# Performance work log

Hardware: AMD Instinct MI355X
Metric: run time of the kernel (lower is better)

The kernel has to match this reference:

```python
import jax, jax.numpy as jnp
import numpy as np

NUM_EXPERTS = 8
TOP_K = 2
B, T, D, F = 4, 2048, 1024, 2816


def setup_inputs() -> dict:
    key = jax.random.key(0)
    ks = jax.random.split(key, 5)
    return {
        "x": jax.random.normal(ks[0], (B, T, D), dtype=jnp.float32),
        "router_w": jax.random.normal(ks[1], (D, NUM_EXPERTS), dtype=jnp.float32) * 0.02,
        "gate_proj": jax.random.normal(ks[2], (NUM_EXPERTS, D, F), dtype=jnp.float32) * 0.02,
        "up_proj": jax.random.normal(ks[3], (NUM_EXPERTS, D, F), dtype=jnp.float32) * 0.02,
        "down_proj": jax.random.normal(ks[4], (NUM_EXPERTS, F, D), dtype=jnp.float32) * 0.02,
    }


def reference(x, router_w, gate_proj, up_proj, down_proj):
    # Router: softmax over experts then top-k (matches original order of ops).
    scores = jnp.einsum('btd,de->bte', x, router_w).astype(jnp.float32)
    probs = jax.nn.softmax(scores, axis=-1)
    routing_weights, routing_idx = jax.lax.top_k(probs, TOP_K)        # (B,T,K)
    routing_weights = (routing_weights / jnp.sum(routing_weights, axis=-1, keepdims=True)).astype(x.dtype)

    # One-hot dispatch mask (B,T,K,E); each expert selected at most once per token.
    one_hot = jax.nn.one_hot(routing_idx, NUM_EXPERTS, dtype=x.dtype)
    # Per-expert combine weight: sum_k mask * w  -> (B,T,E). Same math as the
    # original tiled-mask 'BTED,BTEK->BTD' combine.
    expert_w = jnp.einsum('btke,btk->bte', one_hot, routing_weights)
    # Dense dispatch: x routed (zero-masked) to every expert slot (B,T,E,D),
    # identical to the original 'BTID,BTEK->BTED' einsum.
    dispatched = jnp.einsum('btd,btke->bted', x, one_hot)

    # All-experts SwiGLU MLP (vectorized over the expert axis; same math as the
    # original per-expert Python loop + stack).
    gate = jnp.einsum('bted,edf->btef', dispatched, gate_proj)
    up = jnp.einsum('bted,edf->btef', dispatched, up_proj)
    acts = jax.nn.silu(gate) * up                                      # (B,T,E,F)
    expert_out = jnp.einsum('btef,efd->bted', acts, down_proj)         # (B,T,E,D)

    # Combine with routing weights.
    return jnp.einsum('bted,bte->btd', expert_out, expert_w)
```

## Files before the change

kernel.cpp:

```cpp
#include <hip/hip_runtime.h>

constexpr int TOKENS = 8192;
constexpr int D = 1024;
constexpr int F = 2816;
constexpr int E = 8;

typedef __bf16 bf16x8 __attribute__((ext_vector_type(8)));
typedef float  f32x4  __attribute__((ext_vector_type(4)));

__device__ __forceinline__ unsigned short f32_bf16(float f) {
  union { float f; unsigned u; } v; v.f = f;
  unsigned u = v.u;
  return (unsigned short)((u + 0x7FFFu + ((u >> 16) & 1u)) >> 16);
}

__device__ __forceinline__ void gload_lds16(const void* g, void* l) {
  __builtin_amdgcn_global_load_lds(
      (const __attribute__((address_space(1))) void*)g,
      (__attribute__((address_space(3))) void*)l, 16, 0, 0);
}

__global__ __launch_bounds__(256) void k_transpose(
    const float* __restrict__ src, unsigned short* __restrict__ dst, int R, int C) {
  __shared__ unsigned short tile[64][65];
  const int e = blockIdx.z;
  const int r0 = blockIdx.y * 64, c0 = blockIdx.x * 64;
  const int tid = threadIdx.x;
  const int lr = tid >> 6, lc = tid & 63;
  const float* sp = src + ((size_t)e * R + r0) * C + c0;
  #pragma unroll
  for (int q = 0; q < 16; ++q)
    tile[q*4 + lr][lc] = f32_bf16(sp[(size_t)(q*4 + lr) * C + lc]);
  __syncthreads();
  unsigned short* dp = dst + ((size_t)e * C + c0) * R + r0;
  #pragma unroll
  for (int q = 0; q < 16; ++q)
    dp[(size_t)(q*4 + lr) * R + lc] = tile[lc][q*4 + lr];
}

__global__ __launch_bounds__(256) void k_router(
    const float* __restrict__ x, const float* __restrict__ rw,
    unsigned short* __restrict__ xb,
    int* __restrict__ ltok,
    int* __restrict__ pcode, float* __restrict__ pw,
    int* __restrict__ cnt) {
  const int t = blockIdx.x * 4 + (threadIdx.x >> 6);
  const int l = threadIdx.x & 63;
  const float* xr = x + (size_t)t * D;
  float s0=0,s1=0,s2=0,s3=0,s4=0,s5=0,s6=0,s7=0;
  #pragma unroll
  for (int i = 0; i < D/64; ++i) {
    int d = i*64 + l;
    float xv = xr[d];
    xb[(size_t)t*D + d] = f32_bf16(xv);
    const float4* rp = (const float4*)(rw + d*8);
    float4 a = rp[0], b = rp[1];
    s0 += xv*a.x; s1 += xv*a.y; s2 += xv*a.z; s3 += xv*a.w;
    s4 += xv*b.x; s5 += xv*b.y; s6 += xv*b.z; s7 += xv*b.w;
  }
  float s[8] = {s0,s1,s2,s3,s4,s5,s6,s7};
  #pragma unroll
  for (int e = 0; e < 8; ++e) {
    #pragma unroll
    for (int m = 32; m > 0; m >>= 1) s[e] += __shfl_xor(s[e], m, 64);
  }
  if (l == 0) {
    int i0 = 0; float b0 = s[0];
    #pragma unroll
    for (int e = 1; e < 8; ++e) if (s[e] > b0) { b0 = s[e]; i0 = e; }
    int i1 = (i0 == 0) ? 1 : 0; float b1 = s[i1];
    #pragma unroll
    for (int e = 0; e < 8; ++e) if (e != i0 && s[e] > b1) { b1 = s[e]; i1 = e; }
    float w0 = 1.f / (1.f + __expf(b1 - b0));
    float w1 = 1.f - w0;
    int p0 = atomicAdd(&cnt[i0], 1);
    ltok[i0*TOKENS + p0] = t;
    int p1 = atomicAdd(&cnt[i1], 1);
    ltok[i1*TOKENS + p1] = t;
    pcode[t*2]   = (i0 << 13) | p0;  pw[t*2]   = w0;
    pcode[t*2+1] = (i1 << 13) | p1;  pw[t*2+1] = w1;
  }
}

__global__ void k_scan(const int* __restrict__ cnt, int* __restrict__ offs) {
  if (threadIdx.x == 0) {
    int a = 0;
    for (int e = 0; e < E; ++e) { offs[e] = a; a += cnt[e]; }
    offs[E] = a;
  }
}

__global__ __launch_bounds__(256) void k_pass1(
    const unsigned short* __restrict__ xb,
    const unsigned short* __restrict__ wg,
    const unsigned short* __restrict__ wu,
    const int* __restrict__ ltok,
    const int* __restrict__ cnt,
    const int* __restrict__ offs,
    unsigned short* __restrict__ act) {
  const int e = blockIdx.z;
  const int n = cnt[e];
  const int rt = blockIdx.y;
  if (rt * 128 >= n) return;
  const int ft = blockIdx.x;
  __shared__ unsigned short lA[128*64];
  __shared__ unsigned short lG[128*64];
  __shared__ unsigned short lU[128*64];
  const int tid = threadIdx.x, l = tid & 63, w = tid >> 6;
  const int wr = (w >> 1) * 64, wc = (w & 1) * 64;
  const int sl = (l & 7) ^ ((l >> 3) & 7);
  int tok[4], brow[4];
  #pragma unroll
  for (int q = 0; q < 4; ++q) {
    int r = (w*4 + q)*8 + (l >> 3);
    brow[q] = r;
    int rg = rt*128 + r;
    tok[q] = ltok[e*TOKENS + (rg < n ? rg : 0)];
  }
  f32x4 aG[4][4] = {}; f32x4 aU[4][4] = {};
  for (int k0 = 0; k0 < D; k0 += 64) {
    #pragma unroll
    for (int q = 0; q < 4; ++q) {
      const int dst = (w*4 + q) * 512;
      gload_lds16(xb + (size_t)tok[q]*D + k0 + sl*8, &lA[dst]);
      size_t wo = ((size_t)e*F + ft*128 + brow[q]) * D + k0 + sl*8;
      gload_lds16(wg + wo, &lG[dst]);
      gload_lds16(wu + wo, &lU[dst]);
    }
    __syncthreads();
    #pragma unroll
    for (int ks = 0; ks < 2; ++ks) {
      bf16x8 af[4];
      #pragma unroll
      for (int mi = 0; mi < 4; ++mi) {
        int row = wr + mi*16 + (l & 15);
        int sp  = (ks*4 + (l >> 4)) ^ (row & 7);
        af[mi] = *(const bf16x8*)&lA[row*64 + sp*8];
      }
      #pragma unroll
      for (int ni = 0; ni < 4; ++ni) {
        int fr = wc + ni*16 + (l & 15);
        int sp = (ks*4 + (l >> 4)) ^ (fr & 7);
        bf16x8 bg = *(const bf16x8*)&lG[fr*64 + sp*8];
        bf16x8 bu = *(const bf16x8*)&lU[fr*64 + sp*8];
        #pragma unroll
        for (int mi = 0; mi < 4; ++mi) {
          aG[mi][ni] = __builtin_amdgcn_mfma_f32_16x16x32_bf16(af[mi], bg, aG[mi][ni], 0, 0, 0);
          aU[mi][ni] = __builtin_amdgcn_mfma_f32_16x16x32_bf16(af[mi], bu, aU[mi][ni], 0, 0, 0);
        }
      }
    }
    __syncthreads();
  }
  #pragma unroll
  for (int mi = 0; mi < 4; ++mi) {
    #pragma unroll
    for (int j = 0; j < 4; ++j) {
      int rl = wr + mi*16 + (l >> 4)*4 + j;
      int rg = rt*128 + rl;
      if (rg < n) {
        unsigned short* ap = act + ((size_t)offs[e] + rg) * F + ft*128 + wc + (l & 15);
        #pragma unroll
        for (int ni = 0; ni < 4; ++ni) {
          float g = aG[mi][ni][j], u = aU[mi][ni][j];
          float sv = g / (1.f + __expf(-g)) * u;
          ap[ni*16] = f32_bf16(sv);
        }
      }
    }
  }
}

__global__ __launch_bounds__(256) void k_pass2(
    const unsigned short* __restrict__ act,
    const unsigned short* __restrict__ wdt,
    const int* __restrict__ cnt,
    const int* __restrict__ offs,
    float* __restrict__ eo) {
  const int e = blockIdx.z;
  const int n = cnt[e];
  const int rt = blockIdx.y;
  if (rt * 128 >= n) return;
  const int dt = blockIdx.x;
  __shared__ unsigned short lA[128*64];
  __shared__ unsigned short lB[128*64];
  const int tid = threadIdx.x, l = tid & 63, w = tid >> 6;
  const int wr = (w >> 1) * 64, wc = (w & 1) * 64;
  const int sl = (l & 7) ^ ((l >> 3) & 7);
  size_t arow[4]; int brow[4];
  #pragma unroll
  for (int q = 0; q < 4; ++q) {
    int r = (w*4 + q)*8 + (l >> 3);
    brow[q] = r;
    int rg = rt*128 + r;
    arow[q] = (size_t)offs[e] + (rg < n ? rg : 0);
  }
  f32x4 acc[4][4] = {};
  for (int k0 = 0; k0 < F; k0 += 64) {
    #pragma unroll
    for (int q = 0; q < 4; ++q) {
      const int dst = (w*4 + q) * 512;
      gload_lds16(act + arow[q]*F + k0 + sl*8, &lA[dst]);
      gload_lds16(wdt + ((size_t)e*D + dt*128 + brow[q]) * F + k0 + sl*8, &lB[dst]);
    }
    __syncthreads();
    #pragma unroll
    for (int ks = 0; ks < 2; ++ks) {
      bf16x8 af[4];
      #pragma unroll
      for (int mi = 0; mi < 4; ++mi) {
        int row = wr + mi*16 + (l & 15);
        int sp  = (ks*4 + (l >> 4)) ^ (row & 7);
        af[mi] = *(const bf16x8*)&lA[row*64 + sp*8];
      }
      #pragma unroll
      for (int ni = 0; ni < 4; ++ni) {
        int dr = wc + ni*16 + (l & 15);
        int sp = (ks*4 + (l >> 4)) ^ (dr & 7);
        bf16x8 bd = *(const bf16x8*)&lB[dr*64 + sp*8];
        #pragma unroll
        for (int mi = 0; mi < 4; ++mi)
          acc[mi][ni] = __builtin_amdgcn_mfma_f32_16x16x32_bf16(af[mi], bd, acc[mi][ni], 0, 0, 0);
      }
    }
    __syncthreads();
  }
  #pragma unroll
  for (int mi = 0; mi < 4; ++mi) {
    #pragma unroll
    for (int j = 0; j < 4; ++j) {
      int rl = wr + mi*16 + (l >> 4)*4 + j;
      int rg = rt*128 + rl;
      if (rg < n) {
        float* op = eo + ((size_t)offs[e] + rg) * D + dt*128 + wc + (l & 15);
        #pragma unroll
        for (int ni = 0; ni < 4; ++ni) op[ni*16] = acc[mi][ni][j];
      }
    }
  }
}

__global__ __launch_bounds__(256) void k_combine(
    const float* __restrict__ eo, const int* __restrict__ pcode,
    const float* __restrict__ pw, const int* __restrict__ offs,
    float* __restrict__ out) {
  const int t = blockIdx.x;
  const int d4 = threadIdx.x * 4;
  int c0 = pcode[t*2], c1 = pcode[t*2+1];
  float w0 = pw[t*2], w1 = pw[t*2+1];
  size_t r0 = (size_t)offs[c0 >> 13] + (c0 & 8191);
  size_t r1 = (size_t)offs[c1 >> 13] + (c1 & 8191);
  const float4 a = *(const float4*)&eo[r0*D + d4];
  const float4 b = *(const float4*)&eo[r1*D + d4];
  float4 o;
  o.x = w0*a.x + w1*b.x; o.y = w0*a.y + w1*b.y;
  o.z = w0*a.z + w1*b.z; o.w = w0*a.w + w1*b.w;
  *(float4*)&out[(size_t)t*D + d4] = o;
}

extern "C" void kernel_launch(void* const* d_in, const int* in_sizes, int n_in,
                              void* d_out, int out_size, void* d_ws, size_t ws_size,
                              hipStream_t stream) {
  const float* x  = (const float*)d_in[0];
  const float* rw = (const float*)d_in[1];
  const float* gp = (const float*)d_in[2];
  const float* up = (const float*)d_in[3];
  const float* dp = (const float*)d_in[4];
  float* out = (float*)d_out;
  char* ws = (char*)d_ws;
  size_t off = 0;
  auto take = [&](size_t b) { char* p = ws + off; off += (b + 255) & ~(size_t)255; return p; };
  unsigned short* xb  = (unsigned short*)take((size_t)TOKENS * D * 2);
  unsigned short* wg  = (unsigned short*)take((size_t)E * F * D * 2);
  unsigned short* wu  = (unsigned short*)take((size_t)E * F * D * 2);
  unsigned short* wdt = (unsigned short*)take((size_t)E * D * F * 2);
  unsigned short* act = (unsigned short*)take((size_t)2 * TOKENS * F * 2);
  int*   ltok  = (int*)take((size_t)E * TOKENS * 4);
  int*   pcode = (int*)take((size_t)TOKENS * 2 * 4);
  float* pwv   = (float*)take((size_t)TOKENS * 2 * 4);
  int*   cnt   = (int*)take(64);
  int*   offs  = (int*)take(64);
  float* eo = (float*)wg;

  hipMemsetAsync(cnt, 0, 8 * sizeof(int), stream);
  k_transpose<<<dim3(F/64, D/64, E), 256, 0, stream>>>(gp, wg, D, F);
  k_transpose<<<dim3(F/64, D/64, E), 256, 0, stream>>>(up, wu, D, F);
  k_transpose<<<dim3(D/64, F/64, E), 256, 0, stream>>>(dp, wdt, F, D);
  k_router<<<dim3(TOKENS/4), 256, 0, stream>>>(x, rw, xb, ltok, pcode, pwv, cnt);
  k_scan<<<1, 64, 0, stream>>>(cnt, offs);
  k_pass1<<<dim3(F/128, TOKENS/128, E), 256, 0, stream>>>(xb, wg, wu, ltok, cnt, offs, act);
  k_pass2<<<dim3(D/128, TOKENS/128, E), 256, 0, stream>>>(act, wdt, cnt, offs, eo);
  k_combine<<<dim3(TOKENS), 256, 0, stream>>>(eo, pcode, pwv, offs, out);
}
```

Baseline: 1.030 ms.

## Interleave gate/up weights, double-buffer LDS, enlarge pass1 tiles, fold routing weights

Gate and up projections are transposed into one interleaved weight matrix, so pass1 runs a single 256x256 GEMM tile per 512-thread block. That block keeps gate and up pairs in adjacent accumulator columns for the SiLU epilogue. Both GEMMs double-buffer their LDS stages, prefetching the next K slice while computing the current one, and raise wave priority around the MFMA block. Routing weights are applied in the pass2 epilogue through a per-expert weight list, which reduces combine to a plain add. This uses 128KB of dynamic shared memory and more registers per block, which may limit occupancy.

```diff
diff --git a/kernel.cpp b/kernel.cpp
--- a/kernel.cpp
+++ b/kernel.cpp
@@ -4,6 +4,7 @@
 constexpr int D = 1024;
 constexpr int F = 2816;
 constexpr int E = 8;
+constexpr int NGU = 2 * F;
 
 typedef __bf16 bf16x8 __attribute__((ext_vector_type(8)));
 typedef float  f32x4  __attribute__((ext_vector_type(4)));
@@ -18,6 +19,29 @@
   __builtin_amdgcn_global_load_lds(
       (const __attribute__((address_space(1))) void*)g,
       (__attribute__((address_space(3))) void*)l, 16, 0, 0);
+}
+
+__global__ __launch_bounds__(256) void k_transpose_gu(
+    const float* __restrict__ g, const float* __restrict__ u,
+    unsigned short* __restrict__ wgu) {
+  __shared__ unsigned short tile[64][65];
+  const int e = blockIdx.z;
+  const int d0 = blockIdx.y * 64, f0 = blockIdx.x * 64;
+  const int lr = threadIdx.x >> 6, lc = threadIdx.x & 63;
+  for (int half = 0; half < 2; ++half) {
+    const float* src = (half ? u : g) + ((size_t)e * D + d0) * F + f0;
+    if (half) __syncthreads();
+    #pragma unroll
+    for (int q = 0; q < 16; ++q)
+      tile[lc][q*4 + lr] = f32_bf16(src[(size_t)(q*4 + lr) * F + lc]);
+    __syncthreads();
+    #pragma unroll
+    for (int q = 0; q < 16; ++q) {
+      int fi = q*4 + lr, fg = f0 + fi;
+      int r = (fg >> 4) * 32 + (fg & 15) + half * 16;
+      wgu[((size_t)e * NGU + r) * D + d0 + lc] = tile[fi][lc];
+    }
+  }
 }
 
 __global__ __launch_bounds__(256) void k_transpose(
@@ -25,8 +49,7 @@
   __shared__ unsigned short tile[64][65];
   const int e = blockIdx.z;
   const int r0 = blockIdx.y * 64, c0 = blockIdx.x * 64;
-  const int tid = threadIdx.x;
-  const int lr = tid >> 6, lc = tid & 63;
+  const int lr = threadIdx.x >> 6, lc = threadIdx.x & 63;
   const float* sp = src + ((size_t)e * R + r0) * C + c0;
   #pragma unroll
   for (int q = 0; q < 16; ++q)
@@ -41,8 +64,9 @@
 __global__ __launch_bounds__(256) void k_router(
     const float* __restrict__ x, const float* __restrict__ rw,
     unsigned short* __restrict__ xb,
-    int* __restrict__ ltok,
-    int* __restrict__ pcode, float* __restrict__ pw,
+    unsigned short* __restrict__ ltok,
+    float* __restrict__ lw,
+    int* __restrict__ pcode,
     int* __restrict__ cnt) {
   const int t = blockIdx.x * 4 + (threadIdx.x >> 6);
   const int l = threadIdx.x & 63;
@@ -74,11 +98,13 @@
     float w0 = 1.f / (1.f + __expf(b1 - b0));
     float w1 = 1.f - w0;
     int p0 = atomicAdd(&cnt[i0], 1);
-    ltok[i0*TOKENS + p0] = t;
+    ltok[i0*TOKENS + p0] = (unsigned short)t;
+    lw[i0*TOKENS + p0] = w0;
     int p1 = atomicAdd(&cnt[i1], 1);
-    ltok[i1*TOKENS + p1] = t;
-    pcode[t*2]   = (i0 << 13) | p0;  pw[t*2]   = w0;
-    pcode[t*2+1] = (i1 << 13) | p1;  pw[t*2+1] = w1;
+    ltok[i1*TOKENS + p1] = (unsigned short)t;
+    lw[i1*TOKENS + p1] = w1;
+    pcode[t*2]   = (i0 << 13) | p0;
+    pcode[t*2+1] = (i1 << 13) | p1;
   }
 }
 
@@ -90,90 +116,100 @@
   }
 }
 
-__global__ __launch_bounds__(256) void k_pass1(
+__global__ __launch_bounds__(512, 2) void k_pass1(
     const unsigned short* __restrict__ xb,
-    const unsigned short* __restrict__ wg,
-    const unsigned short* __restrict__ wu,
-    const int* __restrict__ ltok,
+    const unsigned short* __restrict__ wgu,
+    const unsigned short* __restrict__ ltok,
     const int* __restrict__ cnt,
     const int* __restrict__ offs,
     unsigned short* __restrict__ act) {
   const int e = blockIdx.z;
   const int n = cnt[e];
   const int rt = blockIdx.y;
-  if (rt * 128 >= n) return;
+  if (rt * 256 >= n) return;
   const int ft = blockIdx.x;
-  __shared__ unsigned short lA[128*64];
-  __shared__ unsigned short lG[128*64];
-  __shared__ unsigned short lU[128*64];
+  extern __shared__ unsigned short smem[];
   const int tid = threadIdx.x, l = tid & 63, w = tid >> 6;
-  const int wr = (w >> 1) * 64, wc = (w & 1) * 64;
-  const int sl = (l & 7) ^ ((l >> 3) & 7);
-  int tok[4], brow[4];
+  const int wm = w >> 2, wn = w & 3;
+  const int sl = (l & 7) ^ (l >> 3);
+  size_t baseA[4], baseB[4];
+  int dst[4];
   #pragma unroll
   for (int q = 0; q < 4; ++q) {
-    int r = (w*4 + q)*8 + (l >> 3);
-    brow[q] = r;
-    int rg = rt*128 + r;
-    tok[q] = ltok[e*TOKENS + (rg < n ? rg : 0)];
-  }
-  f32x4 aG[4][4] = {}; f32x4 aU[4][4] = {};
-  for (int k0 = 0; k0 < D; k0 += 64) {
-    #pragma unroll
-    for (int q = 0; q < 4; ++q) {
-      const int dst = (w*4 + q) * 512;
-      gload_lds16(xb + (size_t)tok[q]*D + k0 + sl*8, &lA[dst]);
-      size_t wo = ((size_t)e*F + ft*128 + brow[q]) * D + k0 + sl*8;
-      gload_lds16(wg + wo, &lG[dst]);
-      gload_lds16(wu + wo, &lU[dst]);
-    }
+    int r = w*32 + q*8 + (l >> 3);
+    int rg = rt*256 + r;
+    int tok = ltok[e*TOKENS + (rg < n ? rg : 0)];
+    baseA[q] = (size_t)tok * D + sl*8;
+    baseB[q] = ((size_t)e * NGU + ft*256 + r) * D + sl*8;
+    dst[q] = (w*4 + q) * 512;
+  }
+  f32x4 acc[8][4] = {};
+
+  #define P1_STAGE(buf, k0) do { \
+    _Pragma("unroll") \
+    for (int q = 0; q < 4; ++q) { \
+      gload_lds16(xb  + baseA[q] + (k0), &smem[(buf)*32768 + dst[q]]); \
+      gload_lds16(wgu + baseB[q] + (k0), &smem[(buf)*32768 + 16384 + dst[q]]); \
+    } } while (0)
+
+  P1_STAGE(0, 0);
+  __syncthreads();
+  for (int t = 0; t < 16; ++t) {
+    if (t < 15) P1_STAGE((t & 1) ^ 1, (t + 1) * 64);
+    const unsigned short* lA = &smem[(t & 1) * 32768];
+    const unsigned short* lB = lA + 16384;
+    bf16x8 bfr[4][2];
+    #pragma unroll
+    for (int nn = 0; nn < 4; ++nn) {
+      int row = wn*64 + nn*16 + (l & 15);
+      #pragma unroll
+      for (int kk = 0; kk < 2; ++kk) {
+        int sp = (kk*4 + (l >> 4)) ^ (row & 7);
+        bfr[nn][kk] = *(const bf16x8*)&lB[row*64 + sp*8];
+      }
+    }
+    __builtin_amdgcn_s_setprio(1);
+    #pragma unroll
+    for (int m = 0; m < 8; ++m) {
+      int row = wm*128 + m*16 + (l & 15);
+      int sp0 = ((l >> 4)    ) ^ (row & 7);
+      int sp1 = ((l >> 4) + 4) ^ (row & 7);
+      bf16x8 a0 = *(const bf16x8*)&lA[row*64 + sp0*8];
+      bf16x8 a1 = *(const bf16x8*)&lA[row*64 + sp1*8];
+      #pragma unroll
+      for (int nn = 0; nn < 4; ++nn) {
+        acc[m][nn] = __builtin_amdgcn_mfma_f32_16x16x32_bf16(a0, bfr[nn][0], acc[m][nn], 0, 0, 0);
+        acc[m][nn] = __builtin_amdgcn_mfma_f32_16x16x32_bf16(a1, bfr[nn][1], acc[m][nn], 0, 0, 0);
+      }
+    }
+    __builtin_amdgcn_s_setprio(0);
     __syncthreads();
-    #pragma unroll
-    for (int ks = 0; ks < 2; ++ks) {
-      bf16x8 af[4];
-      #pragma unroll
-      for (int mi = 0; mi < 4; ++mi) {
-        int row = wr + mi*16 + (l & 15);
-        int sp  = (ks*4 + (l >> 4)) ^ (row & 7);
-        af[mi] = *(const bf16x8*)&lA[row*64 + sp*8];
-      }
-      #pragma unroll
-      for (int ni = 0; ni < 4; ++ni) {
-        int fr = wc + ni*16 + (l & 15);
-        int sp = (ks*4 + (l >> 4)) ^ (fr & 7);
-        bf16x8 bg = *(const bf16x8*)&lG[fr*64 + sp*8];
-        bf16x8 bu = *(const bf16x8*)&lU[fr*64 + sp*8];
+  }
+  #undef P1_STAGE
+  const int fb0 = ft*8 + wn*2;
+  #pragma unroll
+  for (int m = 0; m < 8; ++m) {
+    #pragma unroll
+    for (int j = 0; j < 4; ++j) {
+      int rl = wm*128 + m*16 + (l >> 4)*4 + j;
+      int rg = rt*256 + rl;
+      if (rg < n) {
+        size_t rowo = ((size_t)offs[e] + rg) * F;
         #pragma unroll
-        for (int mi = 0; mi < 4; ++mi) {
-          aG[mi][ni] = __builtin_amdgcn_mfma_f32_16x16x32_bf16(af[mi], bg, aG[mi][ni], 0, 0, 0);
-          aU[mi][ni] = __builtin_amdgcn_mfma_f32_16x16x32_bf16(af[mi], bu, aU[mi][ni], 0, 0, 0);
+        for (int p = 0; p < 2; ++p) {
+          float g = acc[m][2*p][j], u = acc[m][2*p+1][j];
+          float sv = g / (1.f + __expf(-g)) * u;
+          act[rowo + (size_t)(fb0 + p)*16 + (l & 15)] = f32_bf16(sv);
         }
       }
     }
-    __syncthreads();
-  }
-  #pragma unroll
-  for (int mi = 0; mi < 4; ++mi) {
-    #pragma unroll
-    for (int j = 0; j < 4; ++j) {
-      int rl = wr + mi*16 + (l >> 4)*4 + j;
-      int rg = rt*128 + rl;
-      if (rg < n) {
-        unsigned short* ap = act + ((size_t)offs[e] + rg) * F + ft*128 + wc + (l & 15);
-        #pragma unroll
-        for (int ni = 0; ni < 4; ++ni) {
-          float g = aG[mi][ni][j], u = aU[mi][ni][j];
-          float sv = g / (1.f + __expf(-g)) * u;
-          ap[ni*16] = f32_bf16(sv);
-        }
-      }
-    }
-  }
-}
-
-__global__ __launch_bounds__(256) void k_pass2(
+  }
+}
+
+__global__ __launch_bounds__(256, 2) void k_pass2(
     const unsigned short* __restrict__ act,
     const unsigned short* __restrict__ wdt,
+    const float* __restrict__ lw,
     const int* __restrict__ cnt,
     const int* __restrict__ offs,
     float* __restrict__ eo) {
@@ -182,59 +218,75 @@
   const int rt = blockIdx.y;
   if (rt * 128 >= n) return;
   const int dt = blockIdx.x;
-  __shared__ unsigned short lA[128*64];
-  __shared__ unsigned short lB[128*64];
+  __shared__ unsigned short smem[2][2][8192];
   const int tid = threadIdx.x, l = tid & 63, w = tid >> 6;
   const int wr = (w >> 1) * 64, wc = (w & 1) * 64;
-  const int sl = (l & 7) ^ ((l >> 3) & 7);
-  size_t arow[4]; int brow[4];
+  const int sl = (l & 7) ^ (l >> 3);
+  size_t baseA[4], baseB[4];
+  int dst[4];
   #pragma unroll
   for (int q = 0; q < 4; ++q) {
-    int r = (w*4 + q)*8 + (l >> 3);
-    brow[q] = r;
+    int r = w*32 + q*8 + (l >> 3);
     int rg = rt*128 + r;
-    arow[q] = (size_t)offs[e] + (rg < n ? rg : 0);
+    size_t arow = (size_t)offs[e] + (rg < n ? rg : 0);
+    baseA[q] = arow * F + sl*8;
+    baseB[q] = ((size_t)e * D + dt*128 + r) * F + sl*8;
+    dst[q] = (w*4 + q) * 512;
   }
   f32x4 acc[4][4] = {};
-  for (int k0 = 0; k0 < F; k0 += 64) {
-    #pragma unroll
-    for (int q = 0; q < 4; ++q) {
-      const int dst = (w*4 + q) * 512;
-      gload_lds16(act + arow[q]*F + k0 + sl*8, &lA[dst]);
-      gload_lds16(wdt + ((size_t)e*D + dt*128 + brow[q]) * F + k0 + sl*8, &lB[dst]);
-    }
+
+  #define P2_STAGE(buf, k0) do { \
+    _Pragma("unroll") \
+    for (int q = 0; q < 4; ++q) { \
+      gload_lds16(act + baseA[q] + (k0), &smem[buf][0][dst[q]]); \
+      gload_lds16(wdt + baseB[q] + (k0), &smem[buf][1][dst[q]]); \
+    } } while (0)
+
+  P2_STAGE(0, 0);
+  __syncthreads();
+  for (int t = 0; t < 44; ++t) {
+    if (t < 43) P2_STAGE((t & 1) ^ 1, (t + 1) * 64);
+    const unsigned short* lA = smem[t & 1][0];
+    const unsigned short* lB = smem[t & 1][1];
+    bf16x8 bfr[4][2];
+    #pragma unroll
+    for (int nn = 0; nn < 4; ++nn) {
+      int row = wc + nn*16 + (l & 15);
+      #pragma unroll
+      for (int kk = 0; kk < 2; ++kk) {
+        int sp = (kk*4 + (l >> 4)) ^ (row & 7);
+        bfr[nn][kk] = *(const bf16x8*)&lB[row*64 + sp*8];
+      }
+    }
+    __builtin_amdgcn_s_setprio(1);
+    #pragma unroll
+    for (int m = 0; m < 4; ++m) {
+      int row = wr + m*16 + (l & 15);
+      int sp0 = ((l >> 4)    ) ^ (row & 7);
+      int sp1 = ((l >> 4) + 4) ^ (row & 7);
+      bf16x8 a0 = *(const bf16x8*)&lA[row*64 + sp0*8];
+      bf16x8 a1 = *(const bf16x8*)&lA[row*64 + sp1*8];
+      #pragma unroll
+      for (int nn = 0; nn < 4; ++nn) {
+        acc[m][nn] = __builtin_amdgcn_mfma_f32_16x16x32_bf16(a0, bfr[nn][0], acc[m][nn], 0, 0, 0);
+        acc[m][nn] = __builtin_amdgcn_mfma_f32_16x16x32_bf16(a1, bfr[nn][1], acc[m][nn], 0, 0, 0);
+      }
+    }
+    __builtin_amdgcn_s_setprio(0);
     __syncthreads();
-    #pragma unroll
-    for (int ks = 0; ks < 2; ++ks) {
-      bf16x8 af[4];
-      #pragma unroll
-      for (int mi = 0; mi < 4; ++mi) {
-        int row = wr + mi*16 + (l & 15);
-        int sp  = (ks*4 + (l >> 4)) ^ (row & 7);
-        af[mi] = *(const bf16x8*)&lA[row*64 + sp*8];
-      }
-      #pragma unroll
-      for (int ni = 0; ni < 4; ++ni) {
-        int dr = wc + ni*16 + (l & 15);
-        int sp = (ks*4 + (l >> 4)) ^ (dr & 7);
-        bf16x8 bd = *(const bf16x8*)&lB[dr*64 + sp*8];
-        #pragma unroll
-        for (int mi = 0; mi < 4; ++mi)
-          acc[mi][ni] = __builtin_amdgcn_mfma_f32_16x16x32_bf16(af[mi], bd, acc[mi][ni], 0, 0, 0);
-      }
-    }
-    __syncthreads();
-  }
-  #pragma unroll
-  for (int mi = 0; mi < 4; ++mi) {
+  }
+  #undef P2_STAGE
+  #pragma unroll
+  for (int m = 0; m < 4; ++m) {
     #pragma unroll
     for (int j = 0; j < 4; ++j) {
-      int rl = wr + mi*16 + (l >> 4)*4 + j;
+      int rl = wr + m*16 + (l >> 4)*4 + j;
       int rg = rt*128 + rl;
       if (rg < n) {
+        float wrt = lw[e*TOKENS + rg];
         float* op = eo + ((size_t)offs[e] + rg) * D + dt*128 + wc + (l & 15);
         #pragma unroll
-        for (int ni = 0; ni < 4; ++ni) op[ni*16] = acc[mi][ni][j];
+        for (int nn = 0; nn < 4; ++nn) op[nn*16] = acc[m][nn][j] * wrt;
       }
     }
   }
@@ -242,19 +294,15 @@
 
 __global__ __launch_bounds__(256) void k_combine(
     const float* __restrict__ eo, const int* __restrict__ pcode,
-    const float* __restrict__ pw, const int* __restrict__ offs,
-    float* __restrict__ out) {
+    const int* __restrict__ offs, float* __restrict__ out) {
   const int t = blockIdx.x;
   const int d4 = threadIdx.x * 4;
   int c0 = pcode[t*2], c1 = pcode[t*2+1];
-  float w0 = pw[t*2], w1 = pw[t*2+1];
   size_t r0 = (size_t)offs[c0 >> 13] + (c0 & 8191);
   size_t r1 = (size_t)offs[c1 >> 13] + (c1 & 8191);
   const float4 a = *(const float4*)&eo[r0*D + d4];
   const float4 b = *(const float4*)&eo[r1*D + d4];
-  float4 o;
-  o.x = w0*a.x + w1*b.x; o.y = w0*a.y + w1*b.y;
-  o.z = w0*a.z + w1*b.z; o.w = w0*a.w + w1*b.w;
+  float4 o; o.x = a.x+b.x; o.y = a.y+b.y; o.z = a.z+b.z; o.w = a.w+b.w;
   *(float4*)&out[(size_t)t*D + d4] = o;
 }
 
@@ -271,24 +319,24 @@
   size_t off = 0;
   auto take = [&](size_t b) { char* p = ws + off; off += (b + 255) & ~(size_t)255; return p; };
   unsigned short* xb  = (unsigned short*)take((size_t)TOKENS * D * 2);
-  unsigned short* wg  = (unsigned short*)take((size_t)E * F * D * 2);
-  unsigned short* wu  = (unsigned short*)take((size_t)E * F * D * 2);
+  unsigned short* wgu = (unsigned short*)take((size_t)E * NGU * D * 2);
   unsigned short* wdt = (unsigned short*)take((size_t)E * D * F * 2);
   unsigned short* act = (unsigned short*)take((size_t)2 * TOKENS * F * 2);
-  int*   ltok  = (int*)take((size_t)E * TOKENS * 4);
+  unsigned short* ltok = (unsigned short*)take((size_t)E * TOKENS * 2);
+  float* lw    = (float*)take((size_t)E * TOKENS * 4);
   int*   pcode = (int*)take((size_t)TOKENS * 2 * 4);
-  float* pwv   = (float*)take((size_t)TOKENS * 2 * 4);
   int*   cnt   = (int*)take(64);
   int*   offs  = (int*)take(64);
-  float* eo = (float*)wg;
-
+  float* eo = (float*)wgu;
+
+  (void)hipFuncSetAttribute((const void*)k_pass1,
+                            hipFuncAttributeMaxDynamicSharedMemorySize, 131072);
   hipMemsetAsync(cnt, 0, 8 * sizeof(int), stream);
-  k_transpose<<<dim3(F/64, D/64, E), 256, 0, stream>>>(gp, wg, D, F);
-  k_transpose<<<dim3(F/64, D/64, E), 256, 0, stream>>>(up, wu, D, F);
+  k_transpose_gu<<<dim3(F/64, D/64, E), 256, 0, stream>>>(gp, up, wgu);
   k_transpose<<<dim3(D/64, F/64, E), 256, 0, stream>>>(dp, wdt, F, D);
-  k_router<<<dim3(TOKENS/4), 256, 0, stream>>>(x, rw, xb, ltok, pcode, pwv, cnt);
+  k_router<<<dim3(TOKENS/4), 256, 0, stream>>>(x, rw, xb, ltok, lw, pcode, cnt);
   k_scan<<<1, 64, 0, stream>>>(cnt, offs);
-  k_pass1<<<dim3(F/128, TOKENS/128, E), 256, 0, stream>>>(xb, wg, wu, ltok, cnt, offs, act);
-  k_pass2<<<dim3(D/128, TOKENS/128, E), 256, 0, stream>>>(act, wdt, cnt, offs, eo);
-  k_combine<<<dim3(TOKENS), 256, 0, stream>>>(eo, pcode, pwv, offs, out);
-}
+  k_pass1<<<dim3(NGU/256, TOKENS/256, E), 512, 131072, stream>>>(xb, wgu, ltok, cnt, offs, act);
+  k_pass2<<<dim3(D/128, TOKENS/128, E), 256, 0, stream>>>(act, wdt, lw, cnt, offs, eo);
+  k_combine<<<dim3(TOKENS), 256, 0, stream>>>(eo, pcode, offs, out);
+}
```

Result: faster. 875.5 us (-15.0%).
